# Optimization experiments

Hardware: AMD Instinct MI355X
Metric: run time of the kernel (lower is better)

## Reference

```python
import jax, jax.numpy as jnp
import numpy as np
import math

B, T, H, NH, E, W = 64, 256, 512, 8, 7, 5
DH = H // NH
NEG = -10000.0


def _ln(x, g, b, eps=1e-12):
    m = x.mean(-1, keepdims=True)
    v = ((x - m) ** 2).mean(-1, keepdims=True)
    return (x - m) / jnp.sqrt(v + eps) * g + b


def _attn(q_in, k_in, v_in, Wq, bq, Wk, bk, Wv, bv, bias):
    # q_in: [B,Tq,H], k_in/v_in: [B,Tk,H], bias broadcastable to [B,NH,Tq,Tk]
    Bq, Tq, _ = q_in.shape
    Tk = k_in.shape[1]
    q = (q_in @ Wq + bq).reshape(Bq, Tq, NH, DH)
    k = (k_in @ Wk + bk).reshape(Bq, Tk, NH, DH)
    v = (v_in @ Wv + bv).reshape(Bq, Tk, NH, DH)
    s = jnp.einsum('bqhd,bkhd->bhqk', q, k) / math.sqrt(DH) + bias
    p = jax.nn.softmax(s, axis=-1)
    ctx = jnp.einsum('bhqk,bkhd->bqhd', p, v)
    return ctx.reshape(Bq, Tq, H)


def _make_mask_biases(lengths, speakers):
    # Vectorized equivalents of get_ext_att_mask (additive -10000 biases).
    j = jnp.arange(T)[None, :, None]          # query position
    k = jnp.arange(T)[None, None, :]          # key position
    L = lengths[:, None, None]                # [B,1,1]
    row = j < L                               # valid query rows
    col = k < L                               # valid key cols
    # global: [B,1,1,T], key validity only
    bias_g = ((1.0 - col.astype(jnp.float32)) * NEG)[:, None, :, :]  # j dim acts as the size-1 axis
    # local: sliding window of width W (odd): |j-k| <= W//2, within length
    m_l = row & col & (jnp.abs(j - k) <= (W // 2))
    # intra: same-speaker keys for valid rows (columns NOT trimmed, per source)
    sp_j = speakers[:, :, None]
    sp_k = speakers[:, None, :]
    m_intra = row & (sp_k == sp_j)
    # inter: different-speaker keys for valid rows, columns trimmed to length
    m_inter = row & (sp_k != sp_j) & col
    to_bias = lambda m: ((1.0 - m.astype(jnp.float32)) * NEG)[:, None, :, :]
    return bias_g, to_bias(m_l), to_bias(m_intra), to_bias(m_inter)


def _forward(x, lengths, speakers, emo_table,
             t_Wq, t_bq, t_Wk, t_bk, t_Wv, t_bv, t_Wo, t_bo, t_ln_g, t_ln_b,
             b_Wq, b_bq, b_Wk, b_bk, b_Wv, b_bv, b_Wo, b_bo,
             W1, b1, ln2_g, ln2_b, W2):
    # Tendency attention: utterances attend to the E emotion embeddings (BertAttention)
    emo = jnp.broadcast_to(emo_table[None], (B, E, H))
    ctx = _attn(x, emo, emo, t_Wq, t_bq, t_Wk, t_bk, t_Wv, t_bv, 0.0)
    h_t = _ln(ctx @ t_Wo + t_bo + x, t_ln_g, t_ln_b)
    # Four masked self-attention branches (EmotionAttention: attn + dense, no LN)
    biases = _make_mask_biases(lengths, speakers)
    outs = []
    for i in range(4):
        c = _attn(h_t, h_t, h_t, b_Wq[i], b_bq[i], b_Wk[i], b_bk[i],
                  b_Wv[i], b_bv[i], biases[i])
        outs.append(c @ b_Wo[i] + b_bo[i])
    cat = jnp.concatenate(outs, axis=-1)          # [B,T,4H]
    h_e = _ln(cat @ W1 + b1 + h_t, ln2_g, ln2_b)  # fuse branches + residual + LN
    return h_e @ W2                                # transform2 (no bias)


def setup_inputs():
    key = jax.random.key(0)
    ks = jax.random.split(key, 16)
    nrm = lambda k, shape: jax.random.normal(k, shape, dtype=jnp.float32) * 0.02
    z = lambda *s: jnp.zeros(s, jnp.float32)
    o = lambda *s: jnp.ones(s, jnp.float32)
    return {
        'x': jax.random.normal(ks[0], (B, T, H), dtype=jnp.float32),
        'lengths': jax.random.randint(ks[1], (B,), T // 2, T + 1),
        'speakers': jax.random.randint(ks[2], (B, T), 0, 2),
        'emo_table': nrm(ks[3], (E, H)),
        't_Wq': nrm(ks[4], (H, H)), 't_bq': z(H),
        't_Wk': nrm(ks[5], (H, H)), 't_bk': z(H),
        't_Wv': nrm(ks[6], (H, H)), 't_bv': z(H),
        't_Wo': nrm(ks[7], (H, H)), 't_bo': z(H),
        't_ln_g': o(H), 't_ln_b': z(H),
        'b_Wq': nrm(ks[8], (4, H, H)), 'b_bq': z(4, H),
        'b_Wk': nrm(ks[9], (4, H, H)), 'b_bk': z(4, H),
        'b_Wv': nrm(ks[10], (4, H, H)), 'b_bv': z(4, H),
        'b_Wo': nrm(ks[11], (4, H, H)), 'b_bo': z(4, H),
        'W1': nrm(ks[12], (4 * H, H)), 'b1': z(H),
        'ln2_g': o(H), 'ln2_b': z(H),
        'W2': nrm(ks[13], (H, H)),
    }


def reference(x, lengths, speakers, emo_table,
              t_Wq, t_bq, t_Wk, t_bk, t_Wv, t_bv, t_Wo, t_bo, t_ln_g, t_ln_b,
              b_Wq, b_bq, b_Wk, b_bk, b_Wv, b_bv, b_Wo, b_bo,
              W1, b1, ln2_g, ln2_b, W2):
    return _forward(x, lengths, speakers, emo_table,
                    t_Wq, t_bq, t_Wk, t_bk, t_Wv, t_bv, t_Wo, t_bo, t_ln_g, t_ln_b,
                    b_Wq, b_bq, b_Wk, b_bk, b_Wv, b_bv, b_Wo, b_bo,
                    W1, b1, ln2_g, ln2_b, W2)
```

## Files before the change

### kernel.cpp

```cpp
#include <hip/hip_runtime.h>

#define B_  64
#define T_  256
#define H_  512
#define NH_ 8
#define DH_ 64
#define M_  16384
#define SL  262144

typedef float  f32x4 __attribute__((ext_vector_type(4)));
typedef float  f32x2 __attribute__((ext_vector_type(2)));
typedef __bf16 b16x8 __attribute__((ext_vector_type(8)));
typedef __bf16 b16x4 __attribute__((ext_vector_type(4)));
typedef __bf16 b16x2 __attribute__((ext_vector_type(2)));

__device__ __forceinline__ void gload16(const void* g, void* l) {
  __builtin_amdgcn_global_load_lds((const __attribute__((address_space(1))) void*)g,
                                   (__attribute__((address_space(3))) void*)l, 16, 0, 0);
}

__global__ __launch_bounds__(256) void cvt_f32_bf16_k(const float* __restrict__ in,
                                                      __bf16* __restrict__ out) {
  size_t i = ((size_t)blockIdx.x * 256 + threadIdx.x) * 4;
  f32x4 v = *(const f32x4*)(in + i);
  b16x4 o;
  o[0] = (__bf16)v[0]; o[1] = (__bf16)v[1]; o[2] = (__bf16)v[2]; o[3] = (__bf16)v[3];
  *(b16x4*)(out + i) = o;
}

struct TP15 { const float* src[15]; int slot[15]; float scl[15]; };
__global__ __launch_bounds__(256) void transpose_cvt15(TP15 p, __bf16* __restrict__ wT) {
  __shared__ float tile[32][33];
  const float* in = p.src[blockIdx.z];
  __bf16* out = wT + (size_t)p.slot[blockIdx.z] * SL;
  const float scl = p.scl[blockIdx.z];
  int c0 = blockIdx.x * 32, r0 = blockIdx.y * 32;
  int tx = threadIdx.x & 31, ty = threadIdx.x >> 5;
  for (int yy = ty; yy < 32; yy += 8)
    tile[yy][tx] = in[(size_t)(r0 + yy) * 512 + c0 + tx];
  __syncthreads();
  for (int yy = ty; yy < 32; yy += 8)
    out[(size_t)(c0 + yy) * 512 + r0 + tx] = (__bf16)(tile[tx][yy] * scl);
}

__global__ __launch_bounds__(256) void transpose_cvt(const float* __restrict__ in,
                                                     __bf16* __restrict__ out, int R, int C) {
  __shared__ float tile[32][33];
  int c0 = blockIdx.x * 32, r0 = blockIdx.y * 32;
  int tx = threadIdx.x & 31, ty = threadIdx.x >> 5;
  for (int yy = ty; yy < 32; yy += 8)
    tile[yy][tx] = in[(size_t)(r0 + yy) * C + c0 + tx];
  __syncthreads();
  for (int yy = ty; yy < 32; yy += 8)
    out[(size_t)(c0 + yy) * R + r0 + tx] = (__bf16)tile[tx][yy];
}

__global__ __launch_bounds__(512) void emo_kv(const float* __restrict__ emo,
                                              const float* __restrict__ Wk, const float* __restrict__ bk,
                                              const float* __restrict__ Wv, const float* __restrict__ bv,
                                              float* __restrict__ kout, float* __restrict__ vout) {
  int e = blockIdx.x, n = threadIdx.x;
  const float* W = blockIdx.y ? Wv : Wk;
  const float* bb = blockIdx.y ? bv : bk;
  float* o = blockIdx.y ? vout : kout;
  float acc = 0.f;
  for (int kk = 0; kk < 512; ++kk) acc += emo[e * 512 + kk] * W[kk * 512 + n];
  o[e * 512 + n] = acc + bb[n];
}

__global__ __launch_bounds__(512) void sentprep(const float* __restrict__ Wq,
                                                const float* __restrict__ bq,
                                                const float* __restrict__ Wo,
                                                const float* __restrict__ kemo,
                                                const float* __restrict__ vemo,
                                                __bf16* __restrict__ Wqk_bf,
                                                __bf16* __restrict__ VWo_bf,
                                                float* __restrict__ sbias) {
  const int he = blockIdx.x, h = he / 7, e = he % 7;
  const int t = threadIdx.x;
  const float* kp = kemo + e * 512 + h * 64;
  const float* wqr = Wq + (size_t)t * 512 + h * 64;
  float a = 0.f;
#pragma unroll 8
  for (int d = 0; d < 64; ++d) a += wqr[d] * kp[d];
  Wqk_bf[he * 512 + t] = (__bf16)(a * 0.125f);
  const float* vp = vemo + e * 512 + h * 64;
  float v = 0.f;
#pragma unroll 8
  for (int d = 0; d < 64; ++d) v += vp[d] * Wo[(size_t)(h * 64 + d) * 512 + t];
  VWo_bf[t * 64 + h * 8 + e] = (__bf16)v;
  if (e == 0) VWo_bf[t * 64 + h * 8 + 7] = (__bf16)0.f;
  if (t == 0) {
    float s = 0.f;
    for (int d = 0; d < 64; ++d) s += bq[h * 64 + d] * kp[d];
    sbias[he] = s * 0.125f;
  }
}

__global__ __launch_bounds__(512) void sentpad(__bf16* __restrict__ Wqk_bf,
                                               float* __restrict__ sbias) {
  int r = 56 + blockIdx.x;
  Wqk_bf[r * 512 + threadIdx.x] = (__bf16)0.f;
  if (threadIdx.x == 0) sbias[r] = 0.f;
}

__global__ __launch_bounds__(512) void concat_qk_bias(const float* __restrict__ bq,
                                                      const float* __restrict__ bk,
                                                      float* __restrict__ out) {
  int i = blockIdx.x, t = threadIdx.x;
  out[i * 1024 + t]       = bq[i * 512 + t];
  out[i * 1024 + 512 + t] = bk[i * 512 + t] * 0.125f;
}

__global__ __launch_bounds__(256) void bias2_p1(const float* __restrict__ bo,
                                                const float* __restrict__ W1,
                                                float* __restrict__ partial) {
  int p = blockIdx.x, t = threadIdx.x;
  float a0 = 0.f, a1 = 0.f;
  for (int g = p * 128; g < p * 128 + 128; ++g) {
    float bg = bo[g];
    a0 += bg * W1[(size_t)g * 512 + t];
    a1 += bg * W1[(size_t)g * 512 + 256 + t];
  }
  partial[p * 512 + t] = a0;
  partial[p * 512 + 256 + t] = a1;
}

__global__ __launch_bounds__(256) void bias2_p2(const float* __restrict__ b1,
                                                const float* __restrict__ partial,
                                                float* __restrict__ out) {
  int o = blockIdx.x * 256 + threadIdx.x;
  float acc = b1[o];
#pragma unroll
  for (int p = 0; p < 16; ++p) acc += partial[p * 512 + o];
  out[o] = acc;
}

template<int NF, bool OB, int BM, int SW>
__global__ __launch_bounds__(512, 2) void gemm8p(const __bf16* __restrict__ A,
                                                 const __bf16* __restrict__ Bt,
                                                 const float* __restrict__ bias,
                                                 void* __restrict__ Cv,
                                                 int N, int K, int lda, int ldc) {
  __shared__ __attribute__((aligned(16))) __bf16 As[2][256 * 64];
  __shared__ __attribute__((aligned(16))) __bf16 Bs[2][NF * 64 * 64];
  const int gx = gridDim.x;
  const int bid = blockIdx.y * gx + blockIdx.x;
  int bx, by;
  if (SW == 0) {
    const int nwg = gx * gridDim.y;
    const int cpx = nwg >> 3;
    const int swz = (bid & 7) * cpx + (bid >> 3);
    bx = swz % gx; by = swz / gx;
  } else {
    const int gxc = gx >> 3;
    const int u = bid >> 3, c = bid & 7;
    bx = c * gxc + u % gxc;
    by = u / gxc;
  }
  const int tid = threadIdx.x, lane = tid & 63, wid = tid >> 6;
  const int wr = wid >> 2, wc = wid & 3;
  const int m0 = by * 256, n0 = bx * (NF * 64);
  const int l15 = lane & 15, l16 = lane >> 4;
  const int ra = tid >> 3;
  const int xsl = (tid & 7) ^ (ra & 7);
  const int nt = K >> 6;
  f32x4 acc[8][NF] = {};

#define STAGE8(buf, k0)                                                              \
  { char* aw = (char*)&As[buf][0];                                                   \
    char* bw = (char*)&Bs[buf][0];                                                   \
    _Pragma("unroll")                                                                \
    for (int j = 0; j < 4; ++j)                                                      \
      gload16(A + (size_t)(m0 + j * 64 + ra) * lda + (k0) + xsl * 8,                 \
              aw + (j * 512 + tid) * 16);                                            \
    _Pragma("unroll")                                                                \
    for (int j = 0; j < NF; ++j)                                                     \
      gload16(Bt + (size_t)(n0 + j * 64 + ra) * K + (k0) + xsl * 8,                  \
              bw + (j * 512 + tid) * 16); }

#define CMP8(buf)                                                                    \
  { const char* Ac = (const char*)&As[buf][0];                                       \
    const char* Bc = (const char*)&Bs[buf][0];                                       \
    _Pragma("unroll")                                                                \
    for (int ks = 0; ks < 2; ++ks) {                                                 \
      const int swb = (((ks * 4 + l16) ^ (l15 & 7)) << 4);                           \
      b16x8 af[8], bf[NF];                                                           \
      _Pragma("unroll")                                                              \
      for (int m = 0; m < 8; ++m)                                                    \
        af[m] = *(const b16x8*)(Ac + (wr * 128 + m * 16 + l15) * 128 + swb);         \
      _Pragma("unroll")                                                              \
      for (int n = 0; n < NF; ++n)                                                   \
        bf[n] = *(const b16x8*)(Bc + (wc * (NF * 16) + n * 16 + l15) * 128 + swb);   \
      __builtin_amdgcn_s_setprio(1);                                                 \
      _Pragma("unroll")                                                              \
      for (int m = 0; m < 8; ++m)                                                    \
        _Pragma("unroll")                                                            \
        for (int n = 0; n < NF; ++n)                                                 \
          acc[m][n] = __builtin_amdgcn_mfma_f32_16x16x32_bf16(af[m], bf[n], acc[m][n], 0, 0, 0); \
      __builtin_amdgcn_s_setprio(0);                                                 \
    } }

  STAGE8(0, 0);
  int cur = 0;
  for (int t = 0; t < nt; ++t) {
    if (t + 1 < nt) {
      STAGE8(cur ^ 1, (t + 1) * 64);
      if constexpr (NF == 4) asm volatile("s_waitcnt vmcnt(8)" ::: "memory");
      else                   asm volatile("s_waitcnt vmcnt(6)" ::: "memory");
    } else {
      asm volatile("s_waitcnt vmcnt(0)" ::: "memory");
    }
    __builtin_amdgcn_s_barrier();
    CMP8(cur);
    asm volatile("s_waitcnt lgkmcnt(0)" ::: "memory");
    __builtin_amdgcn_s_barrier();
    cur ^= 1;
  }
#undef STAGE8
#undef CMP8

  const int rb = m0 + wr * 128 + l16 * 4;
  const int cb = n0 + wc * (NF * 16) + l15;
#pragma unroll
  for (int n = 0; n < NF; ++n) {
    int gc = cb + n * 16;
    float bc = (BM == 1) ? bias[gc] : 0.0f;
#pragma unroll
    for (int m = 0; m < 8; ++m) {
#pragma unroll
      for (int rr = 0; rr < 4; ++rr) {
        int gr = rb + m * 16 + rr;
        float val = acc[m][n][rr] + ((BM == 2) ? bias[gr] : bc);
        if (OB) ((__bf16*)Cv)[(size_t)gr * ldc + gc] = (__bf16)val;
        else    ((float*)Cv)[(size_t)gr * ldc + gc] = val;
      }
    }
  }
}

template<bool OB, int BM, int SW>
__global__ __launch_bounds__(256) void gemm_bt64(const __bf16* __restrict__ A,
                                                 const __bf16* __restrict__ Bt,
                                                 const float* __restrict__ bias,
                                                 void* __restrict__ Cv,
                                                 int N, int K, int lda, int ldc,
                                                 size_t zA, size_t zB, size_t zC) {
  __shared__ __attribute__((aligned(16))) __bf16 As[128 * 32];
  __shared__ __attribute__((aligned(16))) __bf16 Bs[64 * 32];
  A  += (size_t)blockIdx.z * zA;
  Bt += (size_t)blockIdx.z * zB;
  char* Cb = (char*)Cv + (size_t)blockIdx.z * zC * (OB ? 2 : 4);
  const int gx = gridDim.x;
  const int bid = blockIdx.y * gx + blockIdx.x;
  int bx, by;
  if (SW == 0) {
    const int nwg = gx * gridDim.y;
    const int cpx = nwg >> 3;
    const int swz = (bid & 7) * cpx + (bid >> 3);
    bx = swz % gx; by = swz / gx;
  } else {
    const int gxc = gx >> 3;
    const int u = bid >> 3, c = bid & 7;
    bx = c * gxc + u % gxc;
    by = u / gxc;
  }
  const int tid = threadIdx.x, lane = tid & 63, wid = tid >> 6;
  const int m0 = by * 128, n0 = bx * 64;
  const int l15 = lane & 15, l16 = lane >> 4;
  const int r0 = tid >> 2, o0 = (tid & 3) * 8;
  const __bf16* a0 = A + (size_t)(m0 + r0) * lda + o0;
  const __bf16* a1 = A + (size_t)(m0 + 64 + r0) * lda + o0;
  const __bf16* bp0 = Bt + (size_t)(n0 + r0) * K + o0;
  char* AsW = (char*)As + wid * 1024;
  char* BsW = (char*)Bs + wid * 1024;
  f32x4 acc[2][4] = {};
  for (int k0 = 0; k0 < K; k0 += 32) {
    gload16(a0 + k0, AsW);
    gload16(a1 + k0, AsW + 4096);
    gload16(bp0 + k0, BsW);
    __syncthreads();
    b16x8 af[2], bf[4];
#pragma unroll
    for (int m = 0; m < 2; ++m) af[m] = *(const b16x8*)&As[(wid * 32 + m * 16 + l15) * 32 + l16 * 8];
#pragma unroll
    for (int n = 0; n < 4; ++n) bf[n] = *(const b16x8*)&Bs[(n * 16 + l15) * 32 + l16 * 8];
#pragma unroll
    for (int m = 0; m < 2; ++m)
#pragma unroll
      for (int n = 0; n < 4; ++n)
        acc[m][n] = __builtin_amdgcn_mfma_f32_16x16x32_bf16(af[m], bf[n], acc[m][n], 0, 0, 0);
    __syncthreads();
  }
  const int rbase = m0 + wid * 32 + l16 * 4;
  const int cb = n0 + l15;
#pragma unroll
  for (int n = 0; n < 4; ++n) {
    int gc = cb + n * 16;
    float bc = (BM == 1) ? bias[gc] : 0.0f;
#pragma unroll
    for (int m = 0; m < 2; ++m) {
#pragma unroll
      for (int rr = 0; rr < 4; ++rr) {
        int gr = rbase + m * 16 + rr;
        float val = acc[m][n][rr] + ((BM == 2) ? bias[gr] : bc);
        if (OB) ((__bf16*)Cb)[(size_t)gr * ldc + gc] = (__bf16)val;
        else    ((float*)Cb)[(size_t)gr * ldc + gc] = val;
      }
    }
  }
}

__global__ __launch_bounds__(256) void softmax7(const float* __restrict__ scores,
                                                __bf16* __restrict__ P) {
  int idx = blockIdx.x * 256 + threadIdx.x;
  int m = idx >> 3, h = idx & 7;
  const float* s = scores + (size_t)m * 64 + h * 7;
  float v[7], mx = -3.4e38f;
#pragma unroll
  for (int e = 0; e < 7; ++e) { v[e] = s[e]; mx = fmaxf(mx, v[e]); }
  float sum = 0.f;
#pragma unroll
  for (int e = 0; e < 7; ++e) { v[e] = __expf(v[e] - mx); sum += v[e]; }
  float inv = 1.f / sum;
  __bf16* o = P + (size_t)m * 64 + h * 8;
#pragma unroll
  for (int e = 0; e < 7; ++e) o[e] = (__bf16)(v[e] * inv);
  o[7] = (__bf16)0.f;
}

__global__ __launch_bounds__(256) void ln1_bf(const __bf16* __restrict__ pre,
                                              const float* __restrict__ res,
                                              const float* __restrict__ g,
                                              const float* __restrict__ bt,
                                              __bf16* __restrict__ ob) {
  int row = blockIdx.x, t = threadIdx.x;
  size_t base = (size_t)row * 512;
  b16x2 p2 = *(const b16x2*)(pre + base + 2 * t);
  f32x2 r2 = *(const f32x2*)(res + base + 2 * t);
  float v0 = (float)p2[0] + r2[0];
  float v1 = (float)p2[1] + r2[1];
  float s = v0 + v1, q = v0 * v0 + v1 * v1;
#pragma unroll
  for (int off = 32; off; off >>= 1) { s += __shfl_xor(s, off); q += __shfl_xor(q, off); }
  __shared__ float ls[4], lq[4];
  int wid = t >> 6, lane = t & 63;
  if (lane == 0) { ls[wid] = s; lq[wid] = q; }
  __syncthreads();
  s = ls[0] + ls[1] + ls[2] + ls[3];
  q = lq[0] + lq[1] + lq[2] + lq[3];
  float mean = s * (1.f / 512.f);
  float var = q * (1.f / 512.f) - mean * mean;
  float rstd = rsqrtf(fmaxf(var, 0.f) + 1e-12f);
  b16x2 o;
  o[0] = (__bf16)((v0 - mean) * rstd * g[2 * t] + bt[2 * t]);
  o[1] = (__bf16)((v1 - mean) * rstd * g[2 * t + 1] + bt[2 * t + 1]);
  *(b16x2*)(ob + base + 2 * t) = o;
}

__global__ __launch_bounds__(256) void ln2_bb(const __bf16* __restrict__ pre,
                                              const __bf16* __restrict__ res,
                                              const float* __restrict__ g,
                                              const float* __restrict__ bt,
                                              __bf16* __restrict__ ob) {
  int row = blockIdx.x, t = threadIdx.x;
  size_t base = (size_t)row * 512;
  b16x2 p2 = *(const b16x2*)(pre + base + 2 * t);
  b16x2 r2 = *(const b16x2*)(res + base + 2 * t);
  float v0 = (float)p2[0] + (float)r2[0];
  float v1 = (float)p2[1] + (float)r2[1];
  float s = v0 + v1, q = v0 * v0 + v1 * v1;
#pragma unroll
  for (int off = 32; off; off >>= 1) { s += __shfl_xor(s, off); q += __shfl_xor(q, off); }
  __shared__ float ls[4], lq[4];
  int wid = t >> 6, lane = t & 63;
  if (lane == 0) { ls[wid] = s; lq[wid] = q; }
  __syncthreads();
  s = ls[0] + ls[1] + ls[2] + ls[3];
  q = lq[0] + lq[1] + lq[2] + lq[3];
  float mean = s * (1.f / 512.f);
  float var = q * (1.f / 512.f) - mean * mean;
  float rstd = rsqrtf(fmaxf(var, 0.f) + 1e-12f);
  b16x2 o;
  o[0] = (__bf16)((v0 - mean) * rstd * g[2 * t] + bt[2 * t]);
  o[1] = (__bf16)((v1 - mean) * rstd * g[2 * t + 1] + bt[2 * t + 1]);
  *(b16x2*)(ob + base + 2 * t) = o;
}

template<int BR>
__global__ __launch_bounds__(256, 4) void attn_branch(const __bf16* __restrict__ q,
                                                      const __bf16* __restrict__ kk_,
                                                      const __bf16* __restrict__ vt,
                                                      __bf16* __restrict__ ctx,
                                                      const int* __restrict__ lengths,
                                                      const int* __restrict__ speakers,
                                                      int sqk, int so) {
  __shared__ __attribute__((aligned(16))) __bf16 Ks[256 * 64];
  __shared__ float redM[2][32];
  __shared__ float redS[2][32];
  __shared__ float rowinv[32];
  __shared__ int spk[256];
  const int tid = threadIdx.x, lane = tid & 63, wid = tid >> 6;
  const int l15 = lane & 15, l16 = lane >> 4;
  const int bh = blockIdx.x, q0 = blockIdx.y * 32;
  const int b = bh >> 3, h = bh & 7;
  const int wq = wid & 1, wk = wid >> 1;
  const int mh = wid & 1, nh = wid >> 1;
  const __bf16* vb2 = vt + (size_t)(h * DH_) * M_ + b * T_;
  const __bf16 CB = (__bf16)10000.0f, mCB = (__bf16)(-10000.0f), ZB = (__bf16)0.0f, OB1 = (__bf16)1.0f;

  {
    const size_t kb0 = (size_t)(b * T_) * sqk + h * DH_;
    const int rsub = lane >> 3, slot = lane & 7;
#pragma unroll
    for (int j = 0; j < 8; ++j) {
      int row = (j * 4 + wid) * 8 + rsub;
      gload16(kk_ + kb0 + (size_t)row * sqk + ((slot ^ (row & 7)) * 8),
              (char*)Ks + (j * 4 + wid) * 1024);
    }
  }
  spk[tid] = speakers[b * T_ + tid];
  b16x8 af0, af1;
  {
    const __bf16* qr = q + (size_t)(b * T_ + q0 + wq * 16 + l15) * sqk + h * DH_;
    af0 = *(const b16x8*)(qr + l16 * 8);
    af1 = *(const b16x8*)(qr + 32 + l16 * 8);
  }
  __syncthreads();

  const int L = lengths[b];
  b16x8 afU = {};
  if (BR != 1 && l16 == 0) {
    int jA = q0 + wq * 16 + l15;
    bool rv = jA < L;
    afU[0] = rv ? OB1 : ZB;
    afU[1] = (rv && spk[jA]) ? OB1 : ZB;
    afU[2] = OB1;
  }

  f32x4 sa[4][2] = {};
#pragma unroll
  for (int kc = 0; kc < 4; ++kc) {
#pragma unroll
    for (int nn = 0; nn < 2; ++nn) {
      int krw = kc * 64 + wk * 32 + nn * 16 + l15;
      b16x8 b0 = *(const b16x8*)((char*)Ks + krw * 128 + ((l16 ^ (krw & 7)) * 16));
      sa[kc][nn] = __builtin_amdgcn_mfma_f32_16x16x32_bf16(af0, b0, sa[kc][nn], 0, 0, 0);
      b16x8 b1 = *(const b16x8*)((char*)Ks + krw * 128 + (((4 + l16) ^ (krw & 7)) * 16));
      sa[kc][nn] = __builtin_amdgcn_mfma_f32_16x16x32_bf16(af1, b1, sa[kc][nn], 0, 0, 0);
      if (BR != 1) {
        b16x8 w = {};
        if (l16 == 0) {
          bool cv = krw < L;
          int sc = spk[krw];
          if (BR == 0) {
            w[2] = cv ? CB : ZB;
          } else if (BR == 2) {
            w[0] = sc ? ZB : CB;
            w[1] = sc ? CB : mCB;
          } else {
            w[0] = (cv && sc) ? CB : ZB;
            w[1] = cv ? (sc ? mCB : CB) : ZB;
          }
        }
        sa[kc][nn] = __builtin_amdgcn_mfma_f32_16x16x32_bf16(afU, w, sa[kc][nn], 0, 0, 0);
      }
    }
  }

  b16x8 vpre[2][2];
#pragma unroll
  for (int kt = 0; kt < 2; ++kt)
#pragma unroll
    for (int n = 0; n < 2; ++n) {
      int d = nh * 32 + n * 16 + l15;
      vpre[kt][n] = *(const b16x8*)(vb2 + (size_t)d * M_ + kt * 32 + l16 * 8);
    }

  const int rloc = wq * 16 + l16 * 4;
  float ev[4][8];
  float mx[4];
#pragma unroll
  for (int rr = 0; rr < 4; ++rr) {
    mx[rr] = -3.4e38f;
    const int j = q0 + rloc + rr;
    const bool rv = j < L;
#pragma unroll
    for (int kc = 0; kc < 4; ++kc)
#pragma unroll
      for (int nn = 0; nn < 2; ++nn) {
        float s;
        if (BR == 1) {
          int c = kc * 64 + wk * 32 + nn * 16 + l15;
          int dj = j - c;
          bool ok = rv && (c < L) && (dj <= 2) && (dj >= -2);
          s = sa[kc][nn][rr] + (ok ? 0.0f : -10000.0f);
        } else {
          s = sa[kc][nn][rr];
        }
        ev[rr][kc * 2 + nn] = s;
        mx[rr] = fmaxf(mx[rr], s);
      }
    mx[rr] = fmaxf(mx[rr], __shfl_xor(mx[rr], 1));
    mx[rr] = fmaxf(mx[rr], __shfl_xor(mx[rr], 2));
    mx[rr] = fmaxf(mx[rr], __shfl_xor(mx[rr], 4));
    mx[rr] = fmaxf(mx[rr], __shfl_xor(mx[rr], 8));
  }
  if (l15 == 0) {
#pragma unroll
    for (int rr = 0; rr < 4; ++rr) redM[wk][rloc + rr] = mx[rr];
  }
  __syncthreads();
  float sm[4];
#pragma unroll
  for (int rr = 0; rr < 4; ++rr) {
    float mxf = fmaxf(redM[0][rloc + rr], redM[1][rloc + rr]);
    float s = 0.f;
#pragma unroll
    for (int i = 0; i < 8; ++i) { float e = __expf(ev[rr][i] - mxf); ev[rr][i] = e; s += e; }
    s += __shfl_xor(s, 1); s += __shfl_xor(s, 2); s += __shfl_xor(s, 4); s += __shfl_xor(s, 8);
    sm[rr] = s;
  }
  if (l15 == 0) {
#pragma unroll
    for (int rr = 0; rr < 4; ++rr) redS[wk][rloc + rr] = sm[rr];
  }
  __syncthreads();
  __bf16* P = (__bf16*)Ks;
#pragma unroll
  for (int rr = 0; rr < 4; ++rr) {
    if (wk == 0 && l15 == 0)
      rowinv[rloc + rr] = 1.0f / (redS[0][rloc + rr] + redS[1][rloc + rr]);
#pragma unroll
    for (int kc = 0; kc < 4; ++kc)
#pragma unroll
      for (int nn = 0; nn < 2; ++nn)
        P[(rloc + rr) * 260 + kc * 64 + wk * 32 + nn * 16 + l15] = (__bf16)ev[rr][kc * 2 + nn];
  }
  __syncthreads();

  f32x4 oa[2] = {};
#pragma unroll
  for (int kt = 0; kt < 8; ++kt) {
    b16x8 afp = *(const b16x8*)(P + (mh * 16 + l15) * 260 + kt * 32 + l16 * 8);
#pragma unroll
    for (int n = 0; n < 2; ++n) {
      b16x8 bfr;
      if (kt < 2) bfr = vpre[kt][n];
      else {
        int d = nh * 32 + n * 16 + l15;
        bfr = *(const b16x8*)(vb2 + (size_t)d * M_ + kt * 32 + l16 * 8);
      }
      oa[n] = __builtin_amdgcn_mfma_f32_16x16x32_bf16(afp, bfr, oa[n], 0, 0, 0);
    }
  }
#pragma unroll
  for (int n = 0; n < 2; ++n)
#pragma unroll
    for (int rr = 0; rr < 4; ++rr) {
      int row = mh * 16 + l16 * 4 + rr;
      ctx[(size_t)(b * T_ + q0 + row) * so + h * DH_ + nh * 32 + n * 16 + l15]
          = (__bf16)(oa[n][rr] * rowinv[row]);
    }
}

extern "C" void kernel_launch(void* const* d_in, const int* in_sizes, int n_in,
                              void* d_out, int out_size, void* d_ws, size_t ws_size,
                              hipStream_t stream) {
  const float* x        = (const float*)d_in[0];
  const int*   lengths  = (const int*)d_in[1];
  const int*   speakers = (const int*)d_in[2];
  const float* emo      = (const float*)d_in[3];
  const float* t_Wq = (const float*)d_in[4];
  const float* t_bq = (const float*)d_in[5];
  const float* t_Wk = (const float*)d_in[6];
  const float* t_bk = (const float*)d_in[7];
  const float* t_Wv = (const float*)d_in[8];
  const float* t_bv = (const float*)d_in[9];
  const float* t_Wo = (const float*)d_in[10];
  const float* t_bo = (const float*)d_in[11];
  const float* t_ln_g = (const float*)d_in[12];
  const float* t_ln_b = (const float*)d_in[13];
  const float* b_Wq = (const float*)d_in[14];
  const float* b_bq = (const float*)d_in[15];
  const float* b_Wk = (const float*)d_in[16];
  const float* b_bk = (const float*)d_in[17];
  const float* b_Wv = (const float*)d_in[18];
  const float* b_bv = (const float*)d_in[19];
  const float* b_Wo = (const float*)d_in[20];
  const float* b_bo = (const float*)d_in[21];
  const float* W1   = (const float*)d_in[22];
  const float* b1   = (const float*)d_in[23];
  const float* ln2_g = (const float*)d_in[24];
  const float* ln2_b = (const float*)d_in[25];
  const float* W2   = (const float*)d_in[26];

  if (ws_size < 232314880) return;

  char* ws = (char*)d_ws;
  __bf16* wT      = (__bf16*)(ws);
  __bf16* bWo_bf  = (__bf16*)(ws + 9437184);
  __bf16* Btbig   = (__bf16*)(ws + 11534336);
  float*  qkbias  = (float*)(ws + 13631488);
  float*  bias2   = (float*)(ws + 13647872);
  float*  kemo    = (float*)(ws + 13649920);
  float*  vemo    = (float*)(ws + 13664256);
  __bf16* Wqk_bf  = (__bf16*)(ws + 13678592);
  __bf16* VWo_bf  = (__bf16*)(ws + 13744128);
  float*  sbias   = (float*)(ws + 13809664);
  __bf16* xb      = (__bf16*)(ws + 13908224);
  __bf16* htb     = (__bf16*)(ws + 30685440);
  __bf16* qkb     = (__bf16*)(ws + 47462656);
  __bf16* vtb_all = (__bf16*)(ws + 81017088);
  __bf16* ctxa    = (__bf16*)(ws + 148125952);
  __bf16* heb  = xb;
  __bf16* tmpb = qkb;
  float*  partial = (float*)qkb;
  float*  scores  = (float*)qkb;
  __bf16* Pmat    = (__bf16*)(ws + 47462656 + 4194304);
  __bf16* sctx    = (__bf16*)(ws + 47462656 + 8388608);

  cvt_f32_bf16_k<<<dim3(8192), 256, 0, stream>>>(x, xb);
  cvt_f32_bf16_k<<<dim3(1024), 256, 0, stream>>>(b_Wo, bWo_bf);
  {
    TP15 p;
    const float* srcs[13] = {b_Wq, b_Wq + SL, b_Wq + 2 * SL, b_Wq + 3 * SL,
                             b_Wk, b_Wk + SL, b_Wk + 2 * SL, b_Wk + 3 * SL,
                             b_Wv, b_Wv + SL, b_Wv + 2 * SL, b_Wv + 3 * SL,
                             W2};
    const int slots[13] = {2, 4, 6, 8, 3, 5, 7, 9, 10, 11, 12, 13, 0};
    for (int i = 0; i < 13; ++i) {
      p.src[i] = srcs[i]; p.slot[i] = slots[i];
      p.scl[i] = (i >= 4 && i < 8) ? 0.125f : 1.0f;
    }
    for (int i = 13; i < 15; ++i) { p.src[i] = W2; p.slot[i] = 0; p.scl[i] = 1.0f; }
    transpose_cvt15<<<dim3(16, 16, 13), 256, 0, stream>>>(p, wT);
  }
  transpose_cvt<<<dim3(16, 64), 256, 0, stream>>>(W1, wT + 14 * SL, 2048, 512);
  emo_kv<<<dim3(7, 2), 512, 0, stream>>>(emo, t_Wk, t_bk, t_Wv, t_bv, kemo, vemo);
  concat_qk_bias<<<dim3(4), 512, 0, stream>>>(b_bq, b_bk, qkbias);
  bias2_p1<<<dim3(16), 256, 0, stream>>>(b_bo, W1, partial);
  bias2_p2<<<dim3(2), 256, 0, stream>>>(b1, partial, bias2);
  sentprep<<<dim3(56), 512, 0, stream>>>(t_Wq, t_bq, t_Wo, kemo, vemo, Wqk_bf, VWo_bf, sbias);
  sentpad<<<dim3(8), 512, 0, stream>>>(Wqk_bf, sbias);
  gemm_bt64<true, 0, 0><<<dim3(8, 4, 4), 256, 0, stream>>>(wT + 14 * SL, bWo_bf, nullptr, Btbig,
                                                           512, 512, 2048, 2048, 512, SL, 512);

  gemm_bt64<false, 1, 0><<<dim3(1, 128), 256, 0, stream>>>(xb, Wqk_bf, sbias, scores,
                                                           64, 512, 512, 64, 0, 0, 0);
  softmax7<<<dim3(512), 256, 0, stream>>>(scores, Pmat);
  gemm_bt64<true, 1, 0><<<dim3(8, 128), 256, 0, stream>>>(Pmat, VWo_bf, t_bo, sctx,
                                                          512, 64, 64, 512, 0, 0, 0);
  ln1_bf<<<dim3(16384), 256, 0, stream>>>(sctx, x, t_ln_g, t_ln_b, htb);

  gemm8p<4, true, 2, 1><<<dim3(64, 8), 512, 0, stream>>>(wT + 10 * SL, htb, b_bv,
                                                         vtb_all, 16384, 512, 512, 16384);

  for (int i = 0; i < 4; ++i) {
    gemm8p<4, true, 1, 0><<<dim3(4, 64), 512, 0, stream>>>(htb, wT + (2 + 2 * i) * SL, qkbias + i * 1024,
                                                           qkb, 1024, 512, 512, 1024);
    dim3 ag(512, 8);
    const __bf16* vti = vtb_all + (size_t)i * 512 * M_;
    switch (i) {
      case 0: attn_branch<0><<<ag, 256, 0, stream>>>(qkb, qkb + 512, vti, ctxa + 0 * 512, lengths, speakers, 1024, 2048); break;
      case 1: attn_branch<1><<<ag, 256, 0, stream>>>(qkb, qkb + 512, vti, ctxa + 1 * 512, lengths, speakers, 1024, 2048); break;
      case 2: attn_branch<2><<<ag, 256, 0, stream>>>(qkb, qkb + 512, vti, ctxa + 2 * 512, lengths, speakers, 1024, 2048); break;
      case 3: attn_branch<3><<<ag, 256, 0, stream>>>(qkb, qkb + 512, vti, ctxa + 3 * 512, lengths, speakers, 1024, 2048); break;
    }
  }

  gemm8p<2, true, 1, 0><<<dim3(4, 64), 512, 0, stream>>>(ctxa, Btbig, bias2, tmpb, 512, 2048, 2048, 512);
  ln2_bb<<<dim3(16384), 256, 0, stream>>>(tmpb, htb, ln2_g, ln2_b, heb);
  gemm8p<2, false, 0, 0><<<dim3(4, 64), 512, 0, stream>>>(heb, wT + 0 * SL, nullptr, (float*)d_out, 512, 512, 512, 512);
}
```

Baseline: 568.1 us.

## Batch two attention branches per QK GEMM and attention launch, use K-32 GEMM tiles

The Q/K projections and the attention kernel now process two branches per launch. The GEMM produces a 2048-wide QK output and the attention kernel picks its branch from blockIdx.z. This halves the number of launches and gives each launch more blocks to fill the GPU. All GEMMs move to a new kernel with a 256x128 tile and a K-step of 32, replacing the K-64 version. That cuts LDS use and staging loads per step, but doubles the barriers per K and lowers MFMA work between syncs. The workspace is re-laid out to hold the wider QK buffer.

```diff
diff --git a/kernel.cpp b/kernel.cpp
--- a/kernel.cpp
+++ b/kernel.cpp
@@ -108,8 +108,9 @@
                                                       const float* __restrict__ bk,
                                                       float* __restrict__ out) {
   int i = blockIdx.x, t = threadIdx.x;
-  out[i * 1024 + t]       = bq[i * 512 + t];
-  out[i * 1024 + 512 + t] = bk[i * 512 + t] * 0.125f;
+  int base = (i >> 1) * 2048 + (i & 1) * 1024;
+  out[base + t]       = bq[i * 512 + t];
+  out[base + 512 + t] = bk[i * 512 + t] * 0.125f;
 }
 
 __global__ __launch_bounds__(256) void bias2_p1(const float* __restrict__ bo,
@@ -136,14 +137,14 @@
   out[o] = acc;
 }
 
-template<int NF, bool OB, int BM, int SW>
-__global__ __launch_bounds__(512, 2) void gemm8p(const __bf16* __restrict__ A,
+template<bool OB, int BM, int SW>
+__global__ __launch_bounds__(512, 2) void gemm32(const __bf16* __restrict__ A,
                                                  const __bf16* __restrict__ Bt,
                                                  const float* __restrict__ bias,
                                                  void* __restrict__ Cv,
                                                  int N, int K, int lda, int ldc) {
-  __shared__ __attribute__((aligned(16))) __bf16 As[2][256 * 64];
-  __shared__ __attribute__((aligned(16))) __bf16 Bs[2][NF * 64 * 64];
+  __shared__ __attribute__((aligned(16))) __bf16 As[2][256 * 32];
+  __shared__ __attribute__((aligned(16))) __bf16 Bs[2][128 * 32];
   const int gx = gridDim.x;
   const int bid = blockIdx.y * gx + blockIdx.x;
   int bx, by;
@@ -160,70 +161,61 @@
   }
   const int tid = threadIdx.x, lane = tid & 63, wid = tid >> 6;
   const int wr = wid >> 2, wc = wid & 3;
-  const int m0 = by * 256, n0 = bx * (NF * 64);
+  const int m0 = by * 256, n0 = bx * 128;
   const int l15 = lane & 15, l16 = lane >> 4;
-  const int ra = tid >> 3;
-  const int xsl = (tid & 7) ^ (ra & 7);
-  const int nt = K >> 6;
-  f32x4 acc[8][NF] = {};
-
-#define STAGE8(buf, k0)                                                              \
+  const int ra = tid >> 2;
+  const int xsl = (tid & 3) ^ ((ra >> 1) & 3);
+  const int nt = K >> 5;
+  f32x4 acc[8][2] = {};
+
+#define STAGE32(buf, k0)                                                             \
   { char* aw = (char*)&As[buf][0];                                                   \
     char* bw = (char*)&Bs[buf][0];                                                   \
-    _Pragma("unroll")                                                                \
-    for (int j = 0; j < 4; ++j)                                                      \
-      gload16(A + (size_t)(m0 + j * 64 + ra) * lda + (k0) + xsl * 8,                 \
-              aw + (j * 512 + tid) * 16);                                            \
-    _Pragma("unroll")                                                                \
-    for (int j = 0; j < NF; ++j)                                                     \
-      gload16(Bt + (size_t)(n0 + j * 64 + ra) * K + (k0) + xsl * 8,                  \
-              bw + (j * 512 + tid) * 16); }
-
-#define CMP8(buf)                                                                    \
+    gload16(A + (size_t)(m0 + ra) * lda + (k0) + xsl * 8, aw + tid * 16);            \
+    gload16(A + (size_t)(m0 + 128 + ra) * lda + (k0) + xsl * 8, aw + (512 + tid) * 16); \
+    gload16(Bt + (size_t)(n0 + ra) * K + (k0) + xsl * 8, bw + tid * 16); }
+
+#define CMP32(buf)                                                                   \
   { const char* Ac = (const char*)&As[buf][0];                                       \
     const char* Bc = (const char*)&Bs[buf][0];                                       \
+    const int swb = ((l16 ^ ((l15 >> 1) & 3)) << 4);                                 \
+    b16x8 af[8], bf[2];                                                              \
     _Pragma("unroll")                                                                \
-    for (int ks = 0; ks < 2; ++ks) {                                                 \
-      const int swb = (((ks * 4 + l16) ^ (l15 & 7)) << 4);                           \
-      b16x8 af[8], bf[NF];                                                           \
+    for (int m = 0; m < 8; ++m)                                                      \
+      af[m] = *(const b16x8*)(Ac + (wr * 128 + m * 16 + l15) * 64 + swb);            \
+    _Pragma("unroll")                                                                \
+    for (int n = 0; n < 2; ++n)                                                      \
+      bf[n] = *(const b16x8*)(Bc + (wc * 32 + n * 16 + l15) * 64 + swb);             \
+    __builtin_amdgcn_s_setprio(1);                                                   \
+    _Pragma("unroll")                                                                \
+    for (int m = 0; m < 8; ++m)                                                      \
       _Pragma("unroll")                                                              \
-      for (int m = 0; m < 8; ++m)                                                    \
-        af[m] = *(const b16x8*)(Ac + (wr * 128 + m * 16 + l15) * 128 + swb);         \
-      _Pragma("unroll")                                                              \
-      for (int n = 0; n < NF; ++n)                                                   \
-        bf[n] = *(const b16x8*)(Bc + (wc * (NF * 16) + n * 16 + l15) * 128 + swb);   \
-      __builtin_amdgcn_s_setprio(1);                                                 \
-      _Pragma("unroll")                                                              \
-      for (int m = 0; m < 8; ++m)                                                    \
-        _Pragma("unroll")                                                            \
-        for (int n = 0; n < NF; ++n)                                                 \
-          acc[m][n] = __builtin_amdgcn_mfma_f32_16x16x32_bf16(af[m], bf[n], acc[m][n], 0, 0, 0); \
-      __builtin_amdgcn_s_setprio(0);                                                 \
-    } }
-
-  STAGE8(0, 0);
+      for (int n = 0; n < 2; ++n)                                                    \
+        acc[m][n] = __builtin_amdgcn_mfma_f32_16x16x32_bf16(af[m], bf[n], acc[m][n], 0, 0, 0); \
+    __builtin_amdgcn_s_setprio(0); }
+
+  STAGE32(0, 0);
   int cur = 0;
   for (int t = 0; t < nt; ++t) {
     if (t + 1 < nt) {
-      STAGE8(cur ^ 1, (t + 1) * 64);
-      if constexpr (NF == 4) asm volatile("s_waitcnt vmcnt(8)" ::: "memory");
-      else                   asm volatile("s_waitcnt vmcnt(6)" ::: "memory");
+      STAGE32(cur ^ 1, (t + 1) * 32);
+      asm volatile("s_waitcnt vmcnt(3)" ::: "memory");
     } else {
       asm volatile("s_waitcnt vmcnt(0)" ::: "memory");
     }
     __builtin_amdgcn_s_barrier();
-    CMP8(cur);
+    CMP32(cur);
     asm volatile("s_waitcnt lgkmcnt(0)" ::: "memory");
     __builtin_amdgcn_s_barrier();
     cur ^= 1;
   }
-#undef STAGE8
-#undef CMP8
+#undef STAGE32
+#undef CMP32
 
   const int rb = m0 + wr * 128 + l16 * 4;
-  const int cb = n0 + wc * (NF * 16) + l15;
-#pragma unroll
-  for (int n = 0; n < NF; ++n) {
+  const int cb = n0 + wc * 32 + l15;
+#pragma unroll
+  for (int n = 0; n < 2; ++n) {
     int gc = cb + n * 16;
     float bc = (BM == 1) ? bias[gc] : 0.0f;
 #pragma unroll
@@ -387,26 +379,30 @@
   *(b16x2*)(ob + base + 2 * t) = o;
 }
 
-template<int BR>
-__global__ __launch_bounds__(256, 4) void attn_branch(const __bf16* __restrict__ q,
-                                                      const __bf16* __restrict__ kk_,
+template<int PAIR>
+__global__ __launch_bounds__(256, 4) void attn_branch(const __bf16* __restrict__ qk,
                                                       const __bf16* __restrict__ vt,
                                                       __bf16* __restrict__ ctx,
                                                       const int* __restrict__ lengths,
-                                                      const int* __restrict__ speakers,
-                                                      int sqk, int so) {
+                                                      const int* __restrict__ speakers) {
   __shared__ __attribute__((aligned(16))) __bf16 Ks[256 * 64];
   __shared__ float redM[2][32];
   __shared__ float redS[2][32];
   __shared__ float rowinv[32];
   __shared__ int spk[256];
+  const int sqk = 2048, so = 2048;
   const int tid = threadIdx.x, lane = tid & 63, wid = tid >> 6;
   const int l15 = lane & 15, l16 = lane >> 4;
   const int bh = blockIdx.x, q0 = blockIdx.y * 32;
+  const int z = blockIdx.z;
+  const int BR = PAIR * 2 + z;
   const int b = bh >> 3, h = bh & 7;
   const int wq = wid & 1, wk = wid >> 1;
   const int mh = wid & 1, nh = wid >> 1;
-  const __bf16* vb2 = vt + (size_t)(h * DH_) * M_ + b * T_;
+  const __bf16* qp = qk + z * 1024;
+  const __bf16* kp = qp + 512;
+  const __bf16* vb2 = vt + (size_t)(BR * 512 + h * DH_) * M_ + b * T_;
+  __bf16* ctxp = ctx + (size_t)BR * 512;
   const __bf16 CB = (__bf16)10000.0f, mCB = (__bf16)(-10000.0f), ZB = (__bf16)0.0f, OB1 = (__bf16)1.0f;
 
   {
@@ -415,14 +411,14 @@
 #pragma unroll
     for (int j = 0; j < 8; ++j) {
       int row = (j * 4 + wid) * 8 + rsub;
-      gload16(kk_ + kb0 + (size_t)row * sqk + ((slot ^ (row & 7)) * 8),
+      gload16(kp + kb0 + (size_t)row * sqk + ((slot ^ (row & 7)) * 8),
               (char*)Ks + (j * 4 + wid) * 1024);
     }
   }
   spk[tid] = speakers[b * T_ + tid];
   b16x8 af0, af1;
   {
-    const __bf16* qr = q + (size_t)(b * T_ + q0 + wq * 16 + l15) * sqk + h * DH_;
+    const __bf16* qr = qp + (size_t)(b * T_ + q0 + wq * 16 + l15) * sqk + h * DH_;
     af0 = *(const b16x8*)(qr + l16 * 8);
     af1 = *(const b16x8*)(qr + 32 + l16 * 8);
   }
@@ -559,7 +555,7 @@
 #pragma unroll
     for (int rr = 0; rr < 4; ++rr) {
       int row = mh * 16 + l16 * 4 + rr;
-      ctx[(size_t)(b * T_ + q0 + row) * so + h * DH_ + nh * 32 + n * 16 + l15]
+      ctxp[(size_t)(b * T_ + q0 + row) * so + h * DH_ + nh * 32 + n * 16 + l15]
           = (__bf16)(oa[n][rr] * rowinv[row]);
     }
 }
@@ -608,17 +604,17 @@
   __bf16* Wqk_bf  = (__bf16*)(ws + 13678592);
   __bf16* VWo_bf  = (__bf16*)(ws + 13744128);
   float*  sbias   = (float*)(ws + 13809664);
-  __bf16* xb      = (__bf16*)(ws + 13908224);
-  __bf16* htb     = (__bf16*)(ws + 30685440);
-  __bf16* qkb     = (__bf16*)(ws + 47462656);
-  __bf16* vtb_all = (__bf16*)(ws + 81017088);
-  __bf16* ctxa    = (__bf16*)(ws + 148125952);
-  __bf16* heb  = xb;
-  __bf16* tmpb = qkb;
-  float*  partial = (float*)qkb;
-  float*  scores  = (float*)qkb;
-  __bf16* Pmat    = (__bf16*)(ws + 47462656 + 4194304);
-  __bf16* sctx    = (__bf16*)(ws + 47462656 + 8388608);
+  __bf16* htb     = (__bf16*)(ws + 13908224);
+  __bf16* qkb2    = (__bf16*)(ws + 30685440);
+  __bf16* vtb_all = (__bf16*)(ws + 97794304);
+  __bf16* ctxa    = (__bf16*)(ws + 164903168);
+  __bf16* xb      = (__bf16*)(ws + 164903168);
+  float*  partial = (float*)(ws + 30685440);
+  float*  scores  = (float*)(ws + 30685440);
+  __bf16* Pmat    = (__bf16*)(ws + 30685440 + 4194304);
+  __bf16* sctx    = (__bf16*)(ws + 30685440 + 8388608);
+  __bf16* tmpb    = qkb2;
+  __bf16* heb     = (__bf16*)(ws + 47462656);
 
   cvt_f32_bf16_k<<<dim3(8192), 256, 0, stream>>>(x, xb);
   cvt_f32_bf16_k<<<dim3(1024), 256, 0, stream>>>(b_Wo, bWo_bf);
@@ -653,23 +649,18 @@
                                                           512, 64, 64, 512, 0, 0, 0);
   ln1_bf<<<dim3(16384), 256, 0, stream>>>(sctx, x, t_ln_g, t_ln_b, htb);
 
-  gemm8p<4, true, 2, 1><<<dim3(64, 8), 512, 0, stream>>>(wT + 10 * SL, htb, b_bv,
-                                                         vtb_all, 16384, 512, 512, 16384);
-
-  for (int i = 0; i < 4; ++i) {
-    gemm8p<4, true, 1, 0><<<dim3(4, 64), 512, 0, stream>>>(htb, wT + (2 + 2 * i) * SL, qkbias + i * 1024,
-                                                           qkb, 1024, 512, 512, 1024);
-    dim3 ag(512, 8);
-    const __bf16* vti = vtb_all + (size_t)i * 512 * M_;
-    switch (i) {
-      case 0: attn_branch<0><<<ag, 256, 0, stream>>>(qkb, qkb + 512, vti, ctxa + 0 * 512, lengths, speakers, 1024, 2048); break;
-      case 1: attn_branch<1><<<ag, 256, 0, stream>>>(qkb, qkb + 512, vti, ctxa + 1 * 512, lengths, speakers, 1024, 2048); break;
-      case 2: attn_branch<2><<<ag, 256, 0, stream>>>(qkb, qkb + 512, vti, ctxa + 2 * 512, lengths, speakers, 1024, 2048); break;
-      case 3: attn_branch<3><<<ag, 256, 0, stream>>>(qkb, qkb + 512, vti, ctxa + 3 * 512, lengths, speakers, 1024, 2048); break;
-    }
-  }
-
-  gemm8p<2, true, 1, 0><<<dim3(4, 64), 512, 0, stream>>>(ctxa, Btbig, bias2, tmpb, 512, 2048, 2048, 512);
+  gemm32<true, 2, 1><<<dim3(128, 8), 512, 0, stream>>>(wT + 10 * SL, htb, b_bv,
+                                                       vtb_all, 16384, 512, 512, 16384);
+
+  for (int p = 0; p < 2; ++p) {
+    gemm32<true, 1, 0><<<dim3(16, 64), 512, 0, stream>>>(htb, wT + (2 + 4 * p) * SL, qkbias + p * 2048,
+                                                         qkb2, 2048, 512, 512, 2048);
+    dim3 ag(512, 8, 2);
+    if (p == 0) attn_branch<0><<<ag, 256, 0, stream>>>(qkb2, vtb_all, ctxa, lengths, speakers);
+    else        attn_branch<1><<<ag, 256, 0, stream>>>(qkb2, vtb_all, ctxa, lengths, speakers);
+  }
+
+  gemm32<true, 1, 0><<<dim3(4, 64), 512, 0, stream>>>(ctxa, Btbig, bias2, tmpb, 512, 2048, 2048, 512);
   ln2_bb<<<dim3(16384), 256, 0, stream>>>(tmpb, htb, ln2_g, ln2_b, heb);
-  gemm8p<2, false, 0, 0><<<dim3(4, 64), 512, 0, stream>>>(heb, wT + 0 * SL, nullptr, (float*)d_out, 512, 512, 512, 512);
-}
+  gemm32<false, 0, 0><<<dim3(4, 64), 512, 0, stream>>>(heb, wT + 0 * SL, nullptr, (float*)d_out, 512, 512, 512, 512);
+}
```

Measured after the change: 567.9 us. About the same (-0.0%).
